# Performance work log

Hardware: AMD Instinct MI355X
Metric: run time of the kernel (lower is better)

Reference implementation:

```python
import jax, jax.numpy as jnp
import numpy as np

E = 2048      # embed_size
H = 16        # heads_size
D_HEAD = E // H          # 128
D_ROPE = 32
SPLIT = D_HEAD - D_ROPE  # 96
C = 512       # d_kv_comp
B, S = 2, 2048
ROT_SCALE = 40.0


def _rotary_emb(seq_len):
    # inv_freq has d_rope//4 entries; emb is [S, d_rope//2]
    half = D_ROPE // 2
    inv_freq = 1.0 / (10000.0 ** (jnp.arange(0, half, 2, dtype=jnp.float32) / half))
    t = jnp.arange(seq_len, dtype=jnp.float32) / ROT_SCALE
    freqs = jnp.einsum('i,j->ij', t, inv_freq)
    return jnp.concatenate([freqs, freqs], axis=-1)  # [S, d_rope//2]


def _rotate_half(x):
    x1, x2 = jnp.split(x, 2, axis=-1)
    return jnp.concatenate([-x2, x1], axis=-1)


def _apply_rotary(x, cos, sin):
    rd = cos.shape[-1]
    x_rot, x_base = x[..., :rd], x[..., rd:]
    x_rot = x_rot * cos + _rotate_half(x_rot) * sin
    return jnp.concatenate([x_rot, x_base], axis=-1)


def setup_inputs() -> dict:
    key = jax.random.key(0)
    ks = jax.random.split(key, 10)

    def xav(k, shape):
        fan_in, fan_out = shape
        lim = float(np.sqrt(6.0 / (fan_in + fan_out)))
        return jax.random.uniform(k, shape, jnp.float32, -lim, lim)

    return {
        'h': jax.random.normal(ks[0], (B, S, E), jnp.float32),
        'W_dkv': xav(ks[1], (E, C)), 'b_dkv': jnp.zeros((C,), jnp.float32),
        'W_dq':  xav(ks[2], (E, C)), 'b_dq':  jnp.zeros((C,), jnp.float32),
        'W_uk':  xav(ks[3], (C, H * SPLIT)),  'b_uk': jnp.zeros((H * SPLIT,), jnp.float32),
        'W_uv':  xav(ks[4], (C, H * D_HEAD)), 'b_uv': jnp.zeros((H * D_HEAD,), jnp.float32),
        'W_uq':  xav(ks[5], (C, H * SPLIT)),  'b_uq': jnp.zeros((H * SPLIT,), jnp.float32),
        'W_qr':  xav(ks[6], (C, H * D_ROPE)), 'b_qr': jnp.zeros((H * D_ROPE,), jnp.float32),
        'W_kr':  xav(ks[7], (E, H * D_ROPE)), 'b_kr': jnp.zeros((H * D_ROPE,), jnp.float32),
        'W_out': xav(ks[8], (H * D_HEAD, E)), 'b_out': jnp.zeros((E,), jnp.float32),
    }


def reference(h, W_dkv, b_dkv, W_dq, b_dq, W_uk, b_uk, W_uv, b_uv,
              W_uq, b_uq, W_qr, b_qr, W_kr, b_kr, W_out, b_out):
    Bq, Sq, _ = h.shape
    c_kv = h @ W_dkv + b_dkv                                   # [B,S,C]
    k = (c_kv @ W_uk + b_uk).reshape(Bq, Sq, H, SPLIT)
    v = (c_kv @ W_uv + b_uv).reshape(Bq, Sq, H, D_HEAD)
    c_q = h @ W_dq + b_dq
    q_base = (c_q @ W_uq + b_uq).reshape(Bq, Sq, H, SPLIT)
    q_rot = (c_q @ W_qr + b_qr).reshape(Bq, Sq, H, D_ROPE)

    emb = _rotary_emb(Sq)                                      # [S, d_rope//2]
    cos = jnp.cos(emb)[None, :, None, :]
    sin = jnp.sin(emb)[None, :, None, :]
    q_rot = _apply_rotary(q_rot, cos, sin)
    k_rot = _apply_rotary((h @ W_kr + b_kr).reshape(Bq, Sq, H, D_ROPE), cos, sin)

    q = jnp.concatenate([q_base, q_rot], axis=-1)              # [B,S,H,d_head]
    k_full = jnp.concatenate([k, k_rot], axis=-1)

    scores = jnp.einsum('bqhd,bkhd->bhqk', q, k_full) / jnp.sqrt(jnp.float32(D_HEAD))
    causal = jnp.tril(jnp.ones((Sq, Sq), dtype=bool))
    scores = jnp.where(causal[None, None], scores, -jnp.inf)
    attn = jax.nn.softmax(scores, axis=-1)
    out = jnp.einsum('bhqk,bkhd->bqhd', attn, v).reshape(Bq, Sq, H * D_HEAD)
    out = out @ W_out + b_out
    return out, c_kv, k_rot
```

## Files before the change

kernel.cpp:

```cpp
#include <hip/hip_runtime.h>
#include <hip/hip_bf16.h>

#define B_   2
#define S_   2048
#define E_   2048
#define H_   16
#define DH_  128
#define DR_  32
#define SP_  96
#define C_   512
#define M_   (B_ * S_)

#define LOG2E 1.4426950408889634f

typedef __attribute__((ext_vector_type(8))) short short8;
typedef __attribute__((ext_vector_type(4))) float floatx4;

__device__ __forceinline__ float bfu(unsigned short u) {
  return __uint_as_float((unsigned)u << 16);
}
__device__ __forceinline__ unsigned short f2bf(float f) {
  unsigned u = __float_as_uint(f);
  return (unsigned short)((u + 0x7fff + ((u >> 16) & 1)) >> 16);
}

__device__ __forceinline__ void gload16(const void* g, void* l) {
  __builtin_amdgcn_global_load_lds(
      (const __attribute__((address_space(1))) void*)g,
      (__attribute__((address_space(3))) void*)l, 16, 0, 0);
}

__global__ __launch_bounds__(256) void f2bf_kernel(
    const float* __restrict__ src, unsigned short* __restrict__ dst) {
  size_t i = ((size_t)blockIdx.x * 256 + threadIdx.x) * 4;
  float4 v = *(const float4*)(src + i);
  ushort4 w;
  w.x = f2bf(v.x); w.y = f2bf(v.y); w.z = f2bf(v.z); w.w = f2bf(v.w);
  *(ushort4*)(dst + i) = w;
}

__global__ __launch_bounds__(256) void transpose_w_kernel(
    const float* __restrict__ W, unsigned short* __restrict__ Wt, int K, int N) {
  __shared__ unsigned short T[32][33];
  int n0 = blockIdx.x * 32, k0 = blockIdx.y * 32;
  int t = threadIdx.x, lane = t & 31, grp = t >> 5;
#pragma unroll
  for (int p = 0; p < 4; p++) {
    int k = p * 8 + grp;
    T[lane][k] = f2bf(W[(size_t)(k0 + k) * N + n0 + lane]);
  }
  __syncthreads();
#pragma unroll
  for (int p = 0; p < 4; p++) {
    int n = p * 8 + grp;
    Wt[(size_t)(n0 + n) * K + k0 + lane] = T[n][lane];
  }
}

struct Seg {
  float* outF;
  unsigned short* outB;
  const float* bias;
  const float* biasM;
  int orow, chunk, gstride, obase, nstart, ileave;
  float oscale;
};

__global__ __launch_bounds__(256) void mfma_gemm(
    const unsigned short* __restrict__ A, const unsigned short* __restrict__ Wt,
    Seg s0, Seg s1, Seg s2, int K) {
  __shared__ unsigned short As0[128 * 32];
  __shared__ unsigned short Bs0[128 * 32];
  __shared__ unsigned short As1[128 * 32];
  __shared__ unsigned short Bs1[128 * 32];
  int tid = threadIdx.x;
  int lane = tid & 63, wave = tid >> 6;
  int l16 = lane & 15, quad = lane >> 4;
  int bm = blockIdx.y * 128, bn = blockIdx.x * 128;
  int wm = (wave & 1) * 64, wn = (wave >> 1) * 64;

  floatx4 acc[4][4];
#pragma unroll
  for (int mt = 0; mt < 4; mt++)
#pragma unroll
    for (int nt = 0; nt < 4; nt++) acc[mt][nt] = (floatx4){0.f, 0.f, 0.f, 0.f};

  int c0 = wave * 2, c1 = c0 + 1;
  int srow = lane >> 2, scol = (lane & 3) * 8;
  const unsigned short* Ag0 = A + (size_t)(bm + c0 * 16 + srow) * K + scol;
  const unsigned short* Ag1 = A + (size_t)(bm + c1 * 16 + srow) * K + scol;
  const unsigned short* Bg0 = Wt + (size_t)(bn + c0 * 16 + srow) * K + scol;
  const unsigned short* Bg1 = Wt + (size_t)(bn + c1 * 16 + srow) * K + scol;

#define GSTAGE(kk, Asb, Bsb) do {            \
    gload16(Ag0 + (kk), &Asb[c0 * 512]);     \
    gload16(Ag1 + (kk), &Asb[c1 * 512]);     \
    gload16(Bg0 + (kk), &Bsb[c0 * 512]);     \
    gload16(Bg1 + (kk), &Bsb[c1 * 512]); } while (0)

#define GCOMPUTE(Asb, Bsb) do {                                            \
    short8 af[4], bfv[4];                                                  \
    _Pragma("unroll")                                                      \
    for (int mt = 0; mt < 4; mt++)                                         \
      af[mt] = *(const short8*)&Asb[(wm + mt * 16 + l16) * 32 + quad * 8]; \
    _Pragma("unroll")                                                      \
    for (int nt = 0; nt < 4; nt++)                                         \
      bfv[nt] = *(const short8*)&Bsb[(wn + nt * 16 + l16) * 32 + quad * 8];\
    _Pragma("unroll")                                                      \
    for (int mt = 0; mt < 4; mt++)                                         \
      _Pragma("unroll")                                                    \
      for (int nt = 0; nt < 4; nt++)                                       \
        acc[mt][nt] = __builtin_amdgcn_mfma_f32_16x16x32_bf16(             \
            af[mt], bfv[nt], acc[mt][nt], 0, 0, 0); } while (0)

  GSTAGE(0, As0, Bs0);
  __syncthreads();
  for (int k0 = 0; k0 < K; k0 += 64) {
    GSTAGE(k0 + 32, As1, Bs1);
    GCOMPUTE(As0, Bs0);
    __syncthreads();
    if (k0 + 64 < K) GSTAGE(k0 + 64, As0, Bs0);
    GCOMPUTE(As1, Bs1);
    __syncthreads();
  }
#undef GSTAGE
#undef GCOMPUTE

  Seg sg = (bn >= s2.nstart) ? s2 : ((bn >= s1.nstart) ? s1 : s0);

#pragma unroll
  for (int mt = 0; mt < 4; mt++) {
    int m0 = bm + wm + mt * 16 + quad * 4;
    float bm4[4] = {0.f, 0.f, 0.f, 0.f};
    if (sg.biasM) {
#pragma unroll
      for (int r = 0; r < 4; r++) bm4[r] = sg.biasM[m0 + r];
    }
#pragma unroll
    for (int nt = 0; nt < 4; nt++) {
      int n = bn + wn + nt * 16 + l16;
      int nl = n - sg.nstart;
      float bv = sg.biasM ? 0.f : sg.bias[nl];
      int ncol = sg.obase + (nl / sg.chunk) * sg.gstride + (nl % sg.chunk);
      if (sg.ileave)
        ncol = (ncol & ~31) | ((ncol & 15) << 1) | ((ncol >> 4) & 1);
#pragma unroll
      for (int r = 0; r < 4; r++) {
        float val = (acc[mt][nt][r] + (sg.biasM ? bm4[r] : bv)) * sg.oscale;
        size_t idx = (size_t)(m0 + r) * sg.orow + ncol;
        if (sg.outF) sg.outF[idx] = val;
        if (sg.outB) sg.outB[idx] = f2bf(val);
      }
    }
  }
}

__global__ __launch_bounds__(256) void rope_kernel(
    unsigned short* __restrict__ qf, unsigned short* __restrict__ kf,
    float* __restrict__ krot_out) {
  int idx = blockIdx.x * 256 + threadIdx.x;
  int j  = idx & 7;
  int h  = (idx >> 3) & (H_ - 1);
  int bs = idx >> 7;
  if (bs >= M_) return;
  int s = bs & (S_ - 1);
  float t = (float)s / 40.0f;
  float ang = t * exp2f(-1.6609640474436813f * (float)j);
  float c = cosf(ang), sn = sinf(ang);

  size_t base = (size_t)bs * 2048 + h * 128 + 96;
  float x0 = bfu(qf[base + j]), x1 = bfu(qf[base + j + 8]);
  qf[base + j]     = f2bf(x0 * c - x1 * sn);
  qf[base + j + 8] = f2bf(x1 * c + x0 * sn);

  float y0 = bfu(kf[base + j]), y1 = bfu(kf[base + j + 8]);
  float r0 = y0 * c - y1 * sn;
  float r1 = y1 * c + y0 * sn;
  kf[base + j]     = f2bf(r0);
  kf[base + j + 8] = f2bf(r1);

  size_t ko = (size_t)bs * (H_ * DR_) + h * DR_;
  krot_out[ko + j]      = r0;
  krot_out[ko + j + 8]  = r1;
  krot_out[ko + 16 + j] = bfu(kf[base + 16 + j]);
  krot_out[ko + 24 + j] = bfu(kf[base + 24 + j]);
}

#define KST 136
#define VST 40
#define PST 40
__global__ __launch_bounds__(256) void attn_kernel(
    const unsigned short* __restrict__ qf, const unsigned short* __restrict__ kf,
    const unsigned short* __restrict__ vt, unsigned short* __restrict__ ao) {
  __shared__ unsigned short Ks[32 * KST];
  __shared__ unsigned short Vs[128 * VST];
  __shared__ unsigned short Ps[4][16 * PST];

  int bid0 = blockIdx.x;
  int xcd  = bid0 & 7;
  int idx  = bid0 >> 3;
  int bh   = xcd * 4 + (idx >> 5);
  int jj   = 31 - (idx & 31);
  int h    = bh & 15;
  int b    = bh >> 4;
  int q0   = jj << 6;

  int tid  = threadIdx.x;
  int wave = tid >> 6;
  int lane = tid & 63;
  int l16  = lane & 15;
  int quad = lane >> 4;

  int srow  = tid >> 3;
  int sd0   = (tid & 7) * 16;
  int vrow  = tid >> 1;
  int vhalf = (tid & 1) * 16;

  int qrow = q0 + wave * 16 + l16;
  const unsigned short* qbase =
      qf + ((size_t)(b * S_ + qrow)) * 2048 + h * 128 + quad * 8;
  short8 qfrag[4];
#pragma unroll
  for (int c = 0; c < 4; c++) qfrag[c] = *(const short8*)(qbase + c * 32);

  floatx4 Oacc[8];
#pragma unroll
  for (int dt = 0; dt < 8; dt++) Oacc[dt] = (floatx4){0.f, 0.f, 0.f, 0.f};
  float lpart[4] = {0.f, 0.f, 0.f, 0.f};

  int qg_lo = q0 + wave * 16;
  int qg_hi = qg_lo + 15;
  int nkt = (q0 >> 5) + 2;

  const unsigned short* kbase =
      kf + ((size_t)(b * S_ + srow)) * 2048 + h * 128 + sd0;
  const unsigned short* vbase =
      vt + ((size_t)(h * 128 + vrow)) * 4096 + b * 2048 + vhalf;
  unsigned short* kd = &Ks[srow * KST + sd0];
  unsigned short* vd = &Vs[vrow * VST + vhalf];

  short8 kr0, kr1, vr0, vr1;
  kr0 = *(const short8*)kbase;
  kr1 = *(const short8*)(kbase + 8);
  vr0 = *(const short8*)vbase;
  vr1 = *(const short8*)(vbase + 8);
  *(short8*)kd = kr0; *(short8*)(kd + 8) = kr1;
  *(short8*)vd = vr0; *(short8*)(vd + 8) = vr1;
  __syncthreads();

  for (int kt = 0; kt < nkt; kt++) {
    bool more = (kt + 1 < nkt);
    if (more) {
      const unsigned short* ks = kbase + (size_t)(kt + 1) * 32 * 2048;
      kr0 = *(const short8*)ks;
      kr1 = *(const short8*)(ks + 8);
      const unsigned short* vs = vbase + (kt + 1) * 32;
      vr0 = *(const short8*)vs;
      vr1 = *(const short8*)(vs + 8);
    }
    int kt0 = kt << 5;
    if (kt0 <= qg_hi) {
      floatx4 s0v = {0.f, 0.f, 0.f, 0.f}, s1v = {0.f, 0.f, 0.f, 0.f};
#pragma unroll
      for (int c = 0; c < 4; c++) {
        short8 kfr = *(const short8*)&Ks[l16 * KST + c * 32 + quad * 8];
        s0v = __builtin_amdgcn_mfma_f32_16x16x32_bf16(qfrag[c], kfr, s0v, 0, 0, 0);
      }
#pragma unroll
      for (int c = 0; c < 4; c++) {
        short8 kfr = *(const short8*)&Ks[(16 + l16) * KST + c * 32 + quad * 8];
        s1v = __builtin_amdgcn_mfma_f32_16x16x32_bf16(qfrag[c], kfr, s1v, 0, 0, 0);
      }

      unsigned short* P = Ps[wave];
      bool diag = (kt0 + 31 > qg_lo);
#pragma unroll
      for (int r = 0; r < 4; r++) {
        float p0 = exp2f(fminf(s0v[r], 80.f));
        float p1 = exp2f(fminf(s1v[r], 80.f));
        if (diag) {
          int q_r = qg_lo + quad * 4 + r;
          if (kt0 + l16 > q_r)      p0 = 0.f;
          if (kt0 + 16 + l16 > q_r) p1 = 0.f;
        }
        unsigned pk;
        asm("v_cvt_pk_bf16_f32 %0, %1, %2" : "=v"(pk) : "v"(p0), "v"(p1));
        *(unsigned*)&P[(quad * 4 + r) * PST + 2 * l16] = pk;
        lpart[r] += p0 + p1;
      }

      short8 pfrag = *(const short8*)&P[l16 * PST + quad * 8];
#pragma unroll
      for (int dt = 0; dt < 8; dt++) {
        short8 vfr = *(const short8*)&Vs[(dt * 16 + l16) * VST + quad * 8];
        Oacc[dt] = __builtin_amdgcn_mfma_f32_16x16x32_bf16(pfrag, vfr, Oacc[dt], 0, 0, 0);
      }
    }
    if (more) {
      __syncthreads();
      *(short8*)kd = kr0; *(short8*)(kd + 8) = kr1;
      *(short8*)vd = vr0; *(short8*)(vd + 8) = vr1;
      __syncthreads();
    }
  }

  float linv[4];
#pragma unroll
  for (int r = 0; r < 4; r++) {
    float ls = lpart[r];
#pragma unroll
    for (int sh = 1; sh < 16; sh <<= 1) ls += __shfl_xor(ls, sh);
    linv[r] = 1.0f / ls;
  }
  int qg = q0 + wave * 16 + quad * 4;
#pragma unroll
  for (int r = 0; r < 4; r++) {
    unsigned short* dst = ao + ((size_t)(b * S_ + qg + r)) * 2048 + h * 128 + l16;
#pragma unroll
    for (int dt = 0; dt < 8; dt++) dst[dt * 16] = f2bf(Oacc[dt][r] * linv[r]);
  }
}

static inline Seg mkseg(float* oF, unsigned short* oB, const float* bias,
                        const float* biasM, int orow, int chunk, int gstride,
                        int obase, int nstart, int ileave, float oscale) {
  Seg s;
  s.outF = oF; s.outB = oB; s.bias = bias; s.biasM = biasM;
  s.orow = orow; s.chunk = chunk; s.gstride = gstride;
  s.obase = obase; s.nstart = nstart; s.ileave = ileave; s.oscale = oscale;
  return s;
}
static inline Seg segnone() {
  return mkseg(nullptr, nullptr, nullptr, nullptr, 1, 1, 1, 0, 0x7fffffff, 0, 1.f);
}

extern "C" void kernel_launch(void* const* d_in, const int* in_sizes, int n_in,
                              void* d_out, int out_size, void* d_ws, size_t ws_size,
                              hipStream_t stream) {
  const float* h     = (const float*)d_in[0];
  const float* W_dkv = (const float*)d_in[1];
  const float* b_dkv = (const float*)d_in[2];
  const float* W_dq  = (const float*)d_in[3];
  const float* b_dq  = (const float*)d_in[4];
  const float* W_uk  = (const float*)d_in[5];
  const float* b_uk  = (const float*)d_in[6];
  const float* W_uv  = (const float*)d_in[7];
  const float* b_uv  = (const float*)d_in[8];
  const float* W_uq  = (const float*)d_in[9];
  const float* b_uq  = (const float*)d_in[10];
  const float* W_qr  = (const float*)d_in[11];
  const float* b_qr  = (const float*)d_in[12];
  const float* W_kr  = (const float*)d_in[13];
  const float* b_kr  = (const float*)d_in[14];
  const float* W_out = (const float*)d_in[15];
  const float* b_out = (const float*)d_in[16];

  float* out      = (float*)d_out;
  float* out_ckv  = out + (size_t)M_ * E_;
  float* out_krot = out_ckv + (size_t)M_ * C_;

  unsigned short* w16 = (unsigned short*)d_ws;
  unsigned short* h_bf   = w16;
  unsigned short* q_bf   = w16 + 8388608;
  unsigned short* k_bf   = w16 + 16777216;
  unsigned short* vt_bf  = w16 + 25165824;
  unsigned short* ao_bf  = w16 + 33554432;
  unsigned short* ckv_bf = w16 + 41943040;
  unsigned short* cq_bf  = w16 + 44040192;
  unsigned short* Wt_dkv = w16 + 46137344;
  unsigned short* Wt_dq  = w16 + 47185920;
  unsigned short* Wt_kr  = w16 + 48234496;
  unsigned short* Wt_uk  = w16 + 49283072;
  unsigned short* Wt_uv  = w16 + 50069504;
  unsigned short* Wt_uq  = w16 + 51118080;
  unsigned short* Wt_qr  = w16 + 51904512;
  unsigned short* Wt_out = w16 + 52166656;

  dim3 blk(256);
  const float qscale = 0.08838834764831845f * LOG2E;

  f2bf_kernel<<<8192, blk, 0, stream>>>(h, h_bf);
  transpose_w_kernel<<<dim3(C_ / 32, E_ / 32), blk, 0, stream>>>(W_dkv, Wt_dkv, E_, C_);
  transpose_w_kernel<<<dim3(C_ / 32, E_ / 32), blk, 0, stream>>>(W_dq, Wt_dq, E_, C_);
  transpose_w_kernel<<<dim3((H_ * DR_) / 32, E_ / 32), blk, 0, stream>>>(W_kr, Wt_kr, E_, H_ * DR_);
  transpose_w_kernel<<<dim3((H_ * SP_) / 32, C_ / 32), blk, 0, stream>>>(W_uk, Wt_uk, C_, H_ * SP_);
  transpose_w_kernel<<<dim3((H_ * DH_) / 32, C_ / 32), blk, 0, stream>>>(W_uv, Wt_uv, C_, H_ * DH_);
  transpose_w_kernel<<<dim3((H_ * SP_) / 32, C_ / 32), blk, 0, stream>>>(W_uq, Wt_uq, C_, H_ * SP_);
  transpose_w_kernel<<<dim3((H_ * DR_) / 32, C_ / 32), blk, 0, stream>>>(W_qr, Wt_qr, C_, H_ * DR_);
  transpose_w_kernel<<<dim3(E_ / 32, E_ / 32), blk, 0, stream>>>(W_out, Wt_out, E_, E_);

  mfma_gemm<<<dim3(1536 / 128, M_ / 128), blk, 0, stream>>>(
      h_bf, Wt_dkv,
      mkseg(out_ckv, ckv_bf, b_dkv, nullptr, C_, C_, C_, 0, 0, 0, 1.f),
      mkseg(nullptr, cq_bf,  b_dq,  nullptr, C_, C_, C_, 0, 512, 0, 1.f),
      mkseg(nullptr, k_bf,   b_kr,  nullptr, 2048, DR_, DH_, SP_, 1024, 0, 1.f),
      E_);
  mfma_gemm<<<dim3((H_ * SP_) / 128, M_ / 128), blk, 0, stream>>>(
      ckv_bf, Wt_uk,
      mkseg(nullptr, k_bf, b_uk, nullptr, 2048, SP_, DH_, 0, 0, 0, 1.f),
      segnone(), segnone(), C_);
  mfma_gemm<<<dim3(M_ / 128, (H_ * DH_) / 128), blk, 0, stream>>>(
      Wt_uv, ckv_bf,
      mkseg(nullptr, vt_bf, nullptr, b_uv, M_, M_, M_, 0, 0, 1, 1.f),
      segnone(), segnone(), C_);
  mfma_gemm<<<dim3(2048 / 128, M_ / 128), blk, 0, stream>>>(
      cq_bf, Wt_uq,
      mkseg(nullptr, q_bf, b_uq, nullptr, 2048, SP_, DH_, 0, 0, 0, qscale),
      mkseg(nullptr, q_bf, b_qr, nullptr, 2048, DR_, DH_, SP_, 1536, 0, qscale),
      segnone(), C_);

  rope_kernel<<<(M_ * H_ * 8) / 256, blk, 0, stream>>>(q_bf, k_bf, out_krot);
  attn_kernel<<<B_ * H_ * 32, blk, 0, stream>>>(q_bf, k_bf, vt_bf, ao_bf);

  mfma_gemm<<<dim3(E_ / 128, M_ / 128), blk, 0, stream>>>(
      ao_bf, Wt_out,
      mkseg(out, nullptr, b_out, nullptr, E_, E_, E_, 0, 0, 0, 1.f),
      segnone(), segnone(), E_);
}
```

Measured before the change: 427.5 us.

## Double-buffer attention tiles, pair causal query blocks, remap GEMM blocks, merge transposes

```diff
diff --git a/kernel.cpp b/kernel.cpp
--- a/kernel.cpp
+++ b/kernel.cpp
@@ -39,10 +39,28 @@
   *(ushort4*)(dst + i) = w;
 }
 
-__global__ __launch_bounds__(256) void transpose_w_kernel(
-    const float* __restrict__ W, unsigned short* __restrict__ Wt, int K, int N) {
+struct TEnt { const float* W; unsigned short* Wt; int K, N, ntiles, nx; };
+struct TTab { TEnt e[8]; };
+
+__global__ __launch_bounds__(256) void transpose_all_kernel(TTab tab) {
   __shared__ unsigned short T[32][33];
-  int n0 = blockIdx.x * 32, k0 = blockIdx.y * 32;
+  int rem = blockIdx.x;
+  const float* W = nullptr; unsigned short* Wt = nullptr;
+  int K = 0, N = 0, nx = 1;
+  bool done = false;
+#pragma unroll
+  for (int j = 0; j < 8; j++) {
+    if (!done) {
+      if (rem < tab.e[j].ntiles) {
+        W = tab.e[j].W; Wt = tab.e[j].Wt;
+        K = tab.e[j].K; N = tab.e[j].N; nx = tab.e[j].nx;
+        done = true;
+      } else {
+        rem -= tab.e[j].ntiles;
+      }
+    }
+  }
+  int n0 = (rem % nx) * 32, k0 = (rem / nx) * 32;
   int t = threadIdx.x, lane = t & 31, grp = t >> 5;
 #pragma unroll
   for (int p = 0; p < 4; p++) {
@@ -76,7 +94,13 @@
   int tid = threadIdx.x;
   int lane = tid & 63, wave = tid >> 6;
   int l16 = lane & 15, quad = lane >> 4;
-  int bm = blockIdx.y * 128, bn = blockIdx.x * 128;
+
+  int gx = gridDim.x;
+  int nwg = gx * gridDim.y;
+  int flat = blockIdx.y * gx + blockIdx.x;
+  int w = (flat & 7) * (nwg >> 3) + (flat >> 3);
+  int by = w / gx, bx = w - by * gx;
+  int bm = by * 128, bn = bx * 128;
   int wm = (wave & 1) * 64, wn = (wave >> 1) * 64;
 
   floatx4 acc[4][4];
@@ -192,18 +216,17 @@
 __global__ __launch_bounds__(256) void attn_kernel(
     const unsigned short* __restrict__ qf, const unsigned short* __restrict__ kf,
     const unsigned short* __restrict__ vt, unsigned short* __restrict__ ao) {
-  __shared__ unsigned short Ks[32 * KST];
-  __shared__ unsigned short Vs[128 * VST];
+  __shared__ unsigned short Ks[2][32 * KST];
+  __shared__ unsigned short Vs[2][128 * VST];
   __shared__ unsigned short Ps[4][16 * PST];
 
   int bid0 = blockIdx.x;
   int xcd  = bid0 & 7;
   int idx  = bid0 >> 3;
-  int bh   = xcd * 4 + (idx >> 5);
-  int jj   = 31 - (idx & 31);
+  int bh   = xcd * 4 + (idx >> 4);
+  int jp   = idx & 15;
   int h    = bh & 15;
   int b    = bh >> 4;
-  int q0   = jj << 6;
 
   int tid  = threadIdx.x;
   int wave = tid >> 6;
@@ -216,109 +239,132 @@
   int vrow  = tid >> 1;
   int vhalf = (tid & 1) * 16;
 
-  int qrow = q0 + wave * 16 + l16;
-  const unsigned short* qbase =
-      qf + ((size_t)(b * S_ + qrow)) * 2048 + h * 128 + quad * 8;
-  short8 qfrag[4];
-#pragma unroll
-  for (int c = 0; c < 4; c++) qfrag[c] = *(const short8*)(qbase + c * 32);
-
-  floatx4 Oacc[8];
-#pragma unroll
-  for (int dt = 0; dt < 8; dt++) Oacc[dt] = (floatx4){0.f, 0.f, 0.f, 0.f};
-  float lpart[4] = {0.f, 0.f, 0.f, 0.f};
-
-  int qg_lo = q0 + wave * 16;
-  int qg_hi = qg_lo + 15;
-  int nkt = (q0 >> 5) + 2;
-
   const unsigned short* kbase =
       kf + ((size_t)(b * S_ + srow)) * 2048 + h * 128 + sd0;
   const unsigned short* vbase =
       vt + ((size_t)(h * 128 + vrow)) * 4096 + b * 2048 + vhalf;
-  unsigned short* kd = &Ks[srow * KST + sd0];
-  unsigned short* vd = &Vs[vrow * VST + vhalf];
-
-  short8 kr0, kr1, vr0, vr1;
-  kr0 = *(const short8*)kbase;
-  kr1 = *(const short8*)(kbase + 8);
-  vr0 = *(const short8*)vbase;
-  vr1 = *(const short8*)(vbase + 8);
-  *(short8*)kd = kr0; *(short8*)(kd + 8) = kr1;
-  *(short8*)vd = vr0; *(short8*)(vd + 8) = vr1;
-  __syncthreads();
-
-  for (int kt = 0; kt < nkt; kt++) {
-    bool more = (kt + 1 < nkt);
-    if (more) {
-      const unsigned short* ks = kbase + (size_t)(kt + 1) * 32 * 2048;
-      kr0 = *(const short8*)ks;
-      kr1 = *(const short8*)(ks + 8);
-      const unsigned short* vs = vbase + (kt + 1) * 32;
-      vr0 = *(const short8*)vs;
-      vr1 = *(const short8*)(vs + 8);
-    }
-    int kt0 = kt << 5;
-    if (kt0 <= qg_hi) {
-      floatx4 s0v = {0.f, 0.f, 0.f, 0.f}, s1v = {0.f, 0.f, 0.f, 0.f};
-#pragma unroll
-      for (int c = 0; c < 4; c++) {
-        short8 kfr = *(const short8*)&Ks[l16 * KST + c * 32 + quad * 8];
-        s0v = __builtin_amdgcn_mfma_f32_16x16x32_bf16(qfrag[c], kfr, s0v, 0, 0, 0);
-      }
-#pragma unroll
-      for (int c = 0; c < 4; c++) {
-        short8 kfr = *(const short8*)&Ks[(16 + l16) * KST + c * 32 + quad * 8];
-        s1v = __builtin_amdgcn_mfma_f32_16x16x32_bf16(qfrag[c], kfr, s1v, 0, 0, 0);
-      }
-
-      unsigned short* P = Ps[wave];
-      bool diag = (kt0 + 31 > qg_lo);
-#pragma unroll
-      for (int r = 0; r < 4; r++) {
-        float p0 = exp2f(fminf(s0v[r], 80.f));
-        float p1 = exp2f(fminf(s1v[r], 80.f));
-        if (diag) {
-          int q_r = qg_lo + quad * 4 + r;
-          if (kt0 + l16 > q_r)      p0 = 0.f;
-          if (kt0 + 16 + l16 > q_r) p1 = 0.f;
-        }
-        unsigned pk;
-        asm("v_cvt_pk_bf16_f32 %0, %1, %2" : "=v"(pk) : "v"(p0), "v"(p1));
-        *(unsigned*)&P[(quad * 4 + r) * PST + 2 * l16] = pk;
-        lpart[r] += p0 + p1;
-      }
-
-      short8 pfrag = *(const short8*)&P[l16 * PST + quad * 8];
-#pragma unroll
-      for (int dt = 0; dt < 8; dt++) {
-        short8 vfr = *(const short8*)&Vs[(dt * 16 + l16) * VST + quad * 8];
-        Oacc[dt] = __builtin_amdgcn_mfma_f32_16x16x32_bf16(pfrag, vfr, Oacc[dt], 0, 0, 0);
-      }
-    }
-    if (more) {
-      __syncthreads();
-      *(short8*)kd = kr0; *(short8*)(kd + 8) = kr1;
-      *(short8*)vd = vr0; *(short8*)(vd + 8) = vr1;
-      __syncthreads();
-    }
-  }
-
-  float linv[4];
-#pragma unroll
-  for (int r = 0; r < 4; r++) {
-    float ls = lpart[r];
-#pragma unroll
-    for (int sh = 1; sh < 16; sh <<= 1) ls += __shfl_xor(ls, sh);
-    linv[r] = 1.0f / ls;
-  }
-  int qg = q0 + wave * 16 + quad * 4;
-#pragma unroll
-  for (int r = 0; r < 4; r++) {
-    unsigned short* dst = ao + ((size_t)(b * S_ + qg + r)) * 2048 + h * 128 + l16;
-#pragma unroll
-    for (int dt = 0; dt < 8; dt++) dst[dt * 16] = f2bf(Oacc[dt][r] * linv[r]);
-  }
+
+#define ACOMPUTE() do {                                                       \
+    int kt0 = t << 5;                                                         \
+    if (kt0 <= qg_hi) {                                                       \
+      const unsigned short* Kc = Ks[cur];                                     \
+      const unsigned short* Vc = Vs[cur];                                     \
+      floatx4 s0v = {0.f,0.f,0.f,0.f}, s1v = {0.f,0.f,0.f,0.f};               \
+      __builtin_amdgcn_s_setprio(1);                                          \
+      _Pragma("unroll")                                                       \
+      for (int c = 0; c < 4; c++) {                                           \
+        short8 kfr = *(const short8*)&Kc[l16 * KST + c * 32 + quad * 8];      \
+        s0v = __builtin_amdgcn_mfma_f32_16x16x32_bf16(qfrag[c], kfr, s0v, 0, 0, 0); \
+      }                                                                       \
+      _Pragma("unroll")                                                       \
+      for (int c = 0; c < 4; c++) {                                           \
+        short8 kfr = *(const short8*)&Kc[(16 + l16) * KST + c * 32 + quad * 8]; \
+        s1v = __builtin_amdgcn_mfma_f32_16x16x32_bf16(qfrag[c], kfr, s1v, 0, 0, 0); \
+      }                                                                       \
+      __builtin_amdgcn_s_setprio(0);                                          \
+      unsigned short* P = Ps[wave];                                           \
+      bool diag = (kt0 + 31 > qg_lo);                                         \
+      _Pragma("unroll")                                                       \
+      for (int r = 0; r < 4; r++) {                                           \
+        float p0 = exp2f(fminf(s0v[r], 80.f));                                \
+        float p1 = exp2f(fminf(s1v[r], 80.f));                                \
+        if (diag) {                                                           \
+          int q_r = qg_lo + quad * 4 + r;                                     \
+          if (kt0 + l16 > q_r)      p0 = 0.f;                                 \
+          if (kt0 + 16 + l16 > q_r) p1 = 0.f;                                 \
+        }                                                                     \
+        unsigned pk;                                                          \
+        asm("v_cvt_pk_bf16_f32 %0, %1, %2" : "=v"(pk) : "v"(p0), "v"(p1));    \
+        *(unsigned*)&P[(quad * 4 + r) * PST + 2 * l16] = pk;                  \
+        lpart[r] += p0 + p1;                                                  \
+      }                                                                       \
+      short8 pfrag = *(const short8*)&P[l16 * PST + quad * 8];                \
+      __builtin_amdgcn_s_setprio(1);                                          \
+      _Pragma("unroll")                                                       \
+      for (int dt = 0; dt < 8; dt++) {                                        \
+        short8 vfr = *(const short8*)&Vc[(dt * 16 + l16) * VST + quad * 8];   \
+        Oacc[dt] = __builtin_amdgcn_mfma_f32_16x16x32_bf16(pfrag, vfr, Oacc[dt], 0, 0, 0); \
+      }                                                                       \
+      __builtin_amdgcn_s_setprio(0);                                          \
+    } } while (0)
+
+#define ABODY(W0, W1, W2, W3, L0, L1, L2, L3) do {                            \
+    unsigned short* kdw = &Ks[cur ^ 1][srow * KST + sd0];                     \
+    unsigned short* vdw = &Vs[cur ^ 1][vrow * VST + vhalf];                   \
+    *(short8*)kdw = W0; *(short8*)(kdw + 8) = W1;                             \
+    *(short8*)vdw = W2; *(short8*)(vdw + 8) = W3;                             \
+    { int tf = (t + 2 < nkt) ? t + 2 : nkt - 1;                               \
+      const unsigned short* ksrc = kbase + (size_t)tf * 65536;                \
+      const unsigned short* vsrc = vbase + tf * 32;                           \
+      L0 = *(const short8*)ksrc; L1 = *(const short8*)(ksrc + 8);             \
+      L2 = *(const short8*)vsrc; L3 = *(const short8*)(vsrc + 8); }           \
+    ACOMPUTE();                                                               \
+    __syncthreads();                                                          \
+    cur ^= 1; } while (0)
+
+  for (int half = 0; half < 2; half++) {
+    int jj = half ? (31 - jp) : jp;
+    int q0 = jj << 6;
+
+    int qrow = q0 + wave * 16 + l16;
+    const unsigned short* qbase =
+        qf + ((size_t)(b * S_ + qrow)) * 2048 + h * 128 + quad * 8;
+    short8 qfrag[4];
+#pragma unroll
+    for (int c = 0; c < 4; c++) qfrag[c] = *(const short8*)(qbase + c * 32);
+
+    floatx4 Oacc[8];
+#pragma unroll
+    for (int dt = 0; dt < 8; dt++) Oacc[dt] = (floatx4){0.f, 0.f, 0.f, 0.f};
+    float lpart[4] = {0.f, 0.f, 0.f, 0.f};
+
+    int qg_lo = q0 + wave * 16;
+    int qg_hi = qg_lo + 15;
+    int nkt = 2 * jj + 2;
+
+    short8 rA0, rA1, rA2, rA3, rB0, rB1, rB2, rB3;
+    rA0 = *(const short8*)kbase;       rA1 = *(const short8*)(kbase + 8);
+    rA2 = *(const short8*)vbase;       rA3 = *(const short8*)(vbase + 8);
+    {
+      unsigned short* kdw = &Ks[0][srow * KST + sd0];
+      unsigned short* vdw = &Vs[0][vrow * VST + vhalf];
+      *(short8*)kdw = rA0; *(short8*)(kdw + 8) = rA1;
+      *(short8*)vdw = rA2; *(short8*)(vdw + 8) = rA3;
+    }
+    {
+      const unsigned short* ksrc = kbase + 65536;
+      const unsigned short* vsrc = vbase + 32;
+      rA0 = *(const short8*)ksrc; rA1 = *(const short8*)(ksrc + 8);
+      rA2 = *(const short8*)vsrc; rA3 = *(const short8*)(vsrc + 8);
+    }
+    __syncthreads();
+
+    int cur = 0, t = 0;
+    while (true) {
+      ABODY(rA0, rA1, rA2, rA3, rB0, rB1, rB2, rB3);
+      if (++t >= nkt) break;
+      ABODY(rB0, rB1, rB2, rB3, rA0, rA1, rA2, rA3);
+      if (++t >= nkt) break;
+    }
+
+    float linv[4];
+#pragma unroll
+    for (int r = 0; r < 4; r++) {
+      float ls = lpart[r];
+#pragma unroll
+      for (int sh = 1; sh < 16; sh <<= 1) ls += __shfl_xor(ls, sh);
+      linv[r] = 1.0f / ls;
+    }
+    int qg = q0 + wave * 16 + quad * 4;
+#pragma unroll
+    for (int r = 0; r < 4; r++) {
+      unsigned short* dst = ao + ((size_t)(b * S_ + qg + r)) * 2048 + h * 128 + l16;
+#pragma unroll
+      for (int dt = 0; dt < 8; dt++) dst[dt * 16] = f2bf(Oacc[dt][r] * linv[r]);
+    }
+  }
+#undef ABODY
+#undef ACOMPUTE
 }
 
 static inline Seg mkseg(float* oF, unsigned short* oB, const float* bias,
@@ -332,6 +378,12 @@
 }
 static inline Seg segnone() {
   return mkseg(nullptr, nullptr, nullptr, nullptr, 1, 1, 1, 0, 0x7fffffff, 0, 1.f);
+}
+static inline TEnt mktent(const float* W, unsigned short* Wt, int K, int N,
+                          int ntiles, int nx) {
+  TEnt e;
+  e.W = W; e.Wt = Wt; e.K = K; e.N = N; e.ntiles = ntiles; e.nx = nx;
+  return e;
 }
 
 extern "C" void kernel_launch(void* const* d_in, const int* in_sizes, int n_in,
@@ -380,14 +432,17 @@
   const float qscale = 0.08838834764831845f * LOG2E;
 
   f2bf_kernel<<<8192, blk, 0, stream>>>(h, h_bf);
-  transpose_w_kernel<<<dim3(C_ / 32, E_ / 32), blk, 0, stream>>>(W_dkv, Wt_dkv, E_, C_);
-  transpose_w_kernel<<<dim3(C_ / 32, E_ / 32), blk, 0, stream>>>(W_dq, Wt_dq, E_, C_);
-  transpose_w_kernel<<<dim3((H_ * DR_) / 32, E_ / 32), blk, 0, stream>>>(W_kr, Wt_kr, E_, H_ * DR_);
-  transpose_w_kernel<<<dim3((H_ * SP_) / 32, C_ / 32), blk, 0, stream>>>(W_uk, Wt_uk, C_, H_ * SP_);
-  transpose_w_kernel<<<dim3((H_ * DH_) / 32, C_ / 32), blk, 0, stream>>>(W_uv, Wt_uv, C_, H_ * DH_);
-  transpose_w_kernel<<<dim3((H_ * SP_) / 32, C_ / 32), blk, 0, stream>>>(W_uq, Wt_uq, C_, H_ * SP_);
-  transpose_w_kernel<<<dim3((H_ * DR_) / 32, C_ / 32), blk, 0, stream>>>(W_qr, Wt_qr, C_, H_ * DR_);
-  transpose_w_kernel<<<dim3(E_ / 32, E_ / 32), blk, 0, stream>>>(W_out, Wt_out, E_, E_);
+
+  TTab tab;
+  tab.e[0] = mktent(W_dkv, Wt_dkv, E_, C_,       1024, 16);
+  tab.e[1] = mktent(W_dq,  Wt_dq,  E_, C_,       1024, 16);
+  tab.e[2] = mktent(W_kr,  Wt_kr,  E_, H_ * DR_, 1024, 16);
+  tab.e[3] = mktent(W_uk,  Wt_uk,  C_, H_ * SP_,  768, 48);
+  tab.e[4] = mktent(W_uv,  Wt_uv,  C_, H_ * DH_, 1024, 64);
+  tab.e[5] = mktent(W_uq,  Wt_uq,  C_, H_ * SP_,  768, 48);
+  tab.e[6] = mktent(W_qr,  Wt_qr,  C_, H_ * DR_,  256, 16);
+  tab.e[7] = mktent(W_out, Wt_out, E_, E_,       4096, 64);
+  transpose_all_kernel<<<9984, blk, 0, stream>>>(tab);
 
   mfma_gemm<<<dim3(1536 / 128, M_ / 128), blk, 0, stream>>>(
       h_bf, Wt_dkv,
@@ -410,7 +465,7 @@
       segnone(), C_);
 
   rope_kernel<<<(M_ * H_ * 8) / 256, blk, 0, stream>>>(q_bf, k_bf, out_krot);
-  attn_kernel<<<B_ * H_ * 32, blk, 0, stream>>>(q_bf, k_bf, vt_bf, ao_bf);
+  attn_kernel<<<B_ * H_ * 16, blk, 0, stream>>>(q_bf, k_bf, vt_bf, ao_bf);
 
   mfma_gemm<<<dim3(E_ / 128, M_ / 128), blk, 0, stream>>>(
       ao_bf, Wt_out,
```

Result: faster. 375.8 us (-12.1%).
